# Performance work log

Measured on AMD Instinct MI355X. Metric: run time of the kernel, lower is better.

## Reference

```python
import jax, jax.numpy as jnp
import numpy as np

# D4 Daubechies filter taps (same filter replicated across all channels)
D4 = jnp.array([0.4829629131445341, 0.8365163037378079, 0.2241438680420134, -0.1294095225512604], dtype=jnp.float32)
N_SCALES = 11
SPARSE_DILATIONS = (512, 1024)


def setup_inputs() -> dict:
    key = jax.random.key(0)
    ks = jax.random.split(key, 12)
    B, N, D, H = 4, 4096, 1024, 16
    s = 0.02
    return {
        "x": jax.random.normal(ks[0], (B, N, D), dtype=jnp.float32),
        "Wqkv": jax.random.normal(ks[1], (D, 3 * D), dtype=jnp.float32) * s,
        "bqkv": jnp.zeros((3 * D,), dtype=jnp.float32),
        "Wout": jax.random.normal(ks[2], (D, D), dtype=jnp.float32) * s,
        "bout": jnp.zeros((D,), dtype=jnp.float32),
        "Wgate": jax.random.normal(ks[3], (D, D), dtype=jnp.float32) * s,
        "bgate": jnp.full((D,), 2.0, dtype=jnp.float32),  # nn.init.constant_(bias, 2.0)
        "scale_gain": jax.random.normal(ks[4], (N_SCALES, H), dtype=jnp.float32) * 0.1,
        "skip_w": jnp.full((len(SPARSE_DILATIONS),), -4.0, dtype=jnp.float32)
                  + jax.random.normal(ks[5], (len(SPARSE_DILATIONS),), dtype=jnp.float32) * 0.1,
        "coupling": jnp.eye(H, dtype=jnp.float32)
                    + 0.01 * jax.random.normal(ks[6], (H, H), dtype=jnp.float32),
    }


def _shift_right(t, s, N):
    """Causal shift along seq axis (axis=2): out[i] = t[i-s], zeros for i < s."""
    if s == 0:
        return t
    return jnp.pad(t, ((0, 0), (0, 0), (s, 0), (0, 0)))[:, :, :N, :]


def reference(x, Wqkv, bqkv, Wout, bout, Wgate, bgate, scale_gain, skip_w, coupling):
    B, N, D = x.shape
    H = scale_gain.shape[1]
    HD = D // H

    qkv = x @ Wqkv + bqkv                       # [B, N, 3D]
    q, k, v = jnp.split(qkv, 3, axis=-1)

    def to_heads(t):
        return t.reshape(B, N, H, HD).transpose(0, 2, 1, 3)  # [B, H, N, HD]

    q, k, v = to_heads(q), to_heads(k), to_heads(v)

    k_mag = jnp.linalg.norm(k, axis=-1, keepdims=True)       # [B, H, N, 1]
    field = v * k_mag                                        # [B, H, N, HD]

    # --- 11-scale causal D4 dilated depthwise conv pyramid ---
    # Depthwise conv with identical filter on every channel == weighted sum of
    # causally shifted copies: y[n] = sum_t D4[t] * field[n - (3-t)*d]
    gains = jax.nn.softmax(scale_gain, axis=0)               # [S, H]
    acc = jnp.zeros_like(field)
    for j in range(scale_gain.shape[0]):
        d = 1 << j
        y = sum(D4[t] * _shift_right(field, (3 - t) * d, N) for t in range(4))
        acc = acc + gains[j][None, :, None, None] * y
    field = acc

    # --- sparse long-distance causal skips (1-tap copies at d=512, 1024) ---
    sw = jax.nn.sigmoid(skip_w)
    skip = sum(sw[i] * _shift_right(field, d, N) for i, d in enumerate(SPARSE_DILATIONS))
    field = field + skip

    # --- gated field coupling across heads ---
    coup = jax.nn.softmax(coupling, axis=-1)                 # [H, H]
    field = jnp.einsum('ij,bjnd->bind', coup, field)

    q_flat = q.transpose(0, 2, 1, 3).reshape(B, N, D)
    gate = jax.nn.sigmoid(q_flat @ Wgate + bgate)
    gathered = field.transpose(0, 2, 1, 3).reshape(B, N, D)
    out = (gathered * gate) @ Wout + bout                    # dropout = identity (eval)
    return out
```

## Files before the change

### kernel.cpp

```cpp
#include <hip/hip_runtime.h>
#include <hip/hip_bf16.h>
#include <math.h>

#define BB 4
#define NSEQ 4096
#define DD 1024
#define HH 16
#define HD 64
#define MROWS (BB * NSEQ)

typedef __attribute__((ext_vector_type(8))) short short8;
typedef float v4f __attribute__((ext_vector_type(4)));
typedef unsigned short u16;

typedef __attribute__((address_space(1))) const void gconst_void;
typedef __attribute__((address_space(3))) void lds_void_t;

__device__ __constant__ int SHIFTS[24] = {0,1,2,3,4,6,8,12,16,24,32,48,64,96,128,192,256,384,512,768,1024,1536,2048,3072};

__device__ inline u16 f2bf(float f) {
    unsigned u = __float_as_uint(f);
    unsigned r = u + 0x7fffu + ((u >> 16) & 1u);
    return (u16)(r >> 16);
}
__device__ inline float bf2f(u16 h) {
    return __uint_as_float(((unsigned)h) << 16);
}
__device__ inline void gl2lds16(const u16* g, u16* l) {
    __builtin_amdgcn_global_load_lds((gconst_void*)g, (lds_void_t*)l, 16, 0, 0);
}

__global__ void prep_kernel(const float* __restrict__ scale_gain, const float* __restrict__ skip_w,
                            const float* __restrict__ coupling, float* __restrict__ coefTab,
                            float* __restrict__ coupS, float* __restrict__ swbuf) {
    const float D4T[4] = {0.4829629131445341f, 0.8365163037378079f, 0.2241438680420134f, -0.1294095225512604f};
    int t = threadIdx.x;
    if (t < 2) swbuf[t] = 1.0f / (1.0f + expf(-skip_w[t]));
    if (t < 16) {
        float m = -1e30f;
        for (int j = 0; j < 16; j++) m = fmaxf(m, coupling[t * 16 + j]);
        float s = 0.f, e[16];
        for (int j = 0; j < 16; j++) { e[j] = expf(coupling[t * 16 + j] - m); s += e[j]; }
        for (int j = 0; j < 16; j++) coupS[t * 16 + j] = e[j] / s;
        float g[11];
        m = -1e30f;
        for (int j = 0; j < 11; j++) m = fmaxf(m, scale_gain[j * 16 + t]);
        s = 0.f;
        for (int j = 0; j < 11; j++) { g[j] = expf(scale_gain[j * 16 + t] - m); s += g[j]; }
        for (int j = 0; j < 11; j++) g[j] /= s;
        float cf[24];
        for (int i = 0; i < 24; i++) cf[i] = 0.f;
        for (int j = 0; j < 11; j++) {
            int d = 1 << j;
            for (int tt = 0; tt < 4; tt++) {
                int sh = (3 - tt) * d;
                for (int i = 0; i < 24; i++) {
                    if (SHIFTS[i] == sh) { cf[i] += g[j] * D4T[tt]; break; }
                }
            }
        }
        for (int i = 0; i < 24; i++) coefTab[t * 24 + i] = cf[i];
    }
}

__global__ __launch_bounds__(256) void bfuse_kernel(const float* __restrict__ bqkv, const float* __restrict__ Wgate,
                                                    const float* __restrict__ bgate, float* __restrict__ bfuse) {
    __shared__ float part[4][64];
    int nloc = threadIdx.x & 63, strip = threadIdx.x >> 6;
    int n = blockIdx.x * 64 + nloc;
    float s = 0.f;
    for (int j = strip * 256; j < strip * 256 + 256; j++)
        s += bqkv[j] * Wgate[(long)j * 1024 + n];
    part[strip][nloc] = s;
    __syncthreads();
    if (strip == 0)
        bfuse[n] = bgate[n] + part[0][nloc] + part[1][nloc] + part[2][nloc] + part[3][nloc];
}

__global__ __launch_bounds__(256) void cast_x_kernel(const float* __restrict__ x, u16* __restrict__ xb) {
    long i = ((long)blockIdx.x * 256 + threadIdx.x) * 8;
    float4 f0 = *(const float4*)&x[i];
    float4 f1 = *(const float4*)&x[i + 4];
    u16 o[8];
    o[0] = f2bf(f0.x); o[1] = f2bf(f0.y); o[2] = f2bf(f0.z); o[3] = f2bf(f0.w);
    o[4] = f2bf(f1.x); o[5] = f2bf(f1.y); o[6] = f2bf(f1.z); o[7] = f2bf(f1.w);
    *(uint4*)&xb[i] = *(uint4*)o;
}

__global__ __launch_bounds__(256) void transpose_cast(const float* __restrict__ W, long ldw,
                                                      u16* __restrict__ WT, long ldt) {
    __shared__ float tile[32][33];
    int tx = threadIdx.x, ty = threadIdx.y;
    long x = (long)blockIdx.x * 32 + tx;
    long y0 = (long)blockIdx.y * 32;
    for (int r = 0; r < 32; r += 8)
        tile[ty + r][tx] = W[(y0 + ty + r) * ldw + x];
    __syncthreads();
    for (int r = 0; r < 32; r += 8)
        WT[((long)blockIdx.x * 32 + ty + r) * ldt + y0 + tx] = f2bf(tile[tx][ty + r]);
}

__global__ __launch_bounds__(256) void cast_q_kernel(const float* __restrict__ Wqkv, u16* __restrict__ WqC) {
    long i = ((long)blockIdx.x * 256 + threadIdx.x) * 4;
    int row = (int)(i >> 10);
    int col = (int)(i & 1023);
    float4 f = *(const float4*)&Wqkv[(long)row * 3072 + col];
    ushort4 o;
    o.x = f2bf(f.x); o.y = f2bf(f.y); o.z = f2bf(f.z); o.w = f2bf(f.w);
    *(ushort4*)&WqC[i] = o;
}

#define GEMM_PRE()                                                                  \
    __shared__ u16 As[128 * 32];                                                    \
    __shared__ u16 Bs[128 * 32];                                                    \
    const int tid = threadIdx.x;                                                    \
    const int wave = tid >> 6, lane = tid & 63;                                     \
    const int wm = wave >> 1, wn = wave & 1;                                        \
    const int lrow = lane & 15, kq = lane >> 4;                                     \
    const long m0 = (long)blockIdx.y * 128, n0 = (long)blockIdx.x * 128;            \
    const int r0 = wave * 32 + (lane >> 2);                                         \
    const int sg = (lane & 3) ^ ((r0 >> 1) & 3);                                    \
    const u16* a0 = A + (m0 + r0) * lda + sg * 8;                                   \
    const u16* a1 = a0 + 16 * lda;                                                  \
    const u16* b0 = BT + (n0 + r0) * ldb + sg * 8;                                  \
    const u16* b1 = b0 + 16 * ldb;                                                  \
    u16* la0 = &As[(wave * 32) * 32];                                               \
    u16* la1 = &As[(wave * 32 + 16) * 32];                                          \
    u16* lb0 = &Bs[(wave * 32) * 32];                                               \
    u16* lb1 = &Bs[(wave * 32 + 16) * 32];                                          \
    const int acol = (kq ^ ((lrow >> 1) & 3)) * 8;                                  \
    v4f acc[4][4];                                                                  \
    _Pragma("unroll") for (int i = 0; i < 4; i++)                                   \
        _Pragma("unroll") for (int j = 0; j < 4; j++)                               \
            acc[i][j] = (v4f){0.f, 0.f, 0.f, 0.f};                                  \
    for (int k0 = 0; k0 < K; k0 += 32) {                                            \
        gl2lds16(a0 + k0, la0);                                                     \
        gl2lds16(a1 + k0, la1);                                                     \
        gl2lds16(b0 + k0, lb0);                                                     \
        gl2lds16(b1 + k0, lb1);                                                     \
        __syncthreads();                                                            \
        short8 af[4], bf[4];                                                        \
        _Pragma("unroll") for (int i = 0; i < 4; i++)                               \
            af[i] = *(const short8*)&As[(wm * 64 + i * 16 + lrow) * 32 + acol];     \
        _Pragma("unroll") for (int i = 0; i < 4; i++)                               \
            bf[i] = *(const short8*)&Bs[(wn * 64 + i * 16 + lrow) * 32 + acol];     \
        _Pragma("unroll") for (int im = 0; im < 4; im++)                            \
            _Pragma("unroll") for (int in = 0; in < 4; in++)                        \
                acc[im][in] = __builtin_amdgcn_mfma_f32_16x16x32_bf16(af[im], bf[in], acc[im][in], 0, 0, 0); \
        __syncthreads();                                                            \
    }

template <int CMODE>
__global__ __launch_bounds__(256) void gemm2(const u16* __restrict__ A, long lda,
                                             const u16* __restrict__ BT, long ldb, int K,
                                             const float* __restrict__ bias,
                                             void* __restrict__ Cptr, long ldc) {
    GEMM_PRE()
#pragma unroll
    for (int im = 0; im < 4; im++) {
#pragma unroll
        for (int in = 0; in < 4; in++) {
            long row = m0 + wm * 64 + im * 16 + kq * 4;
            long col = n0 + wn * 64 + in * 16 + lrow;
            float bv = bias ? bias[col] : 0.f;
#pragma unroll
            for (int i = 0; i < 4; i++) {
                float val = acc[im][in][i] + bv;
                long idx = (row + i) * ldc + col;
                if (CMODE == 0) ((float*)Cptr)[idx] = val;
                else            ((u16*)Cptr)[idx] = f2bf(val);
            }
        }
    }
}

#define WAITV(N) asm volatile("s_waitcnt vmcnt(" #N ")" ::: "memory")

template <int CMODE>
__global__ __launch_bounds__(512, 2) void gemm256(const u16* __restrict__ A, long lda,
                                                  const u16* __restrict__ BT, long ldb, int K,
                                                  const float* __restrict__ bias,
                                                  const float* __restrict__ bias2,
                                                  void* __restrict__ C0, void* __restrict__ C1,
                                                  long ldc) {
    __shared__ u16 smem[4 * 2 * 8192];
    const int tid = threadIdx.x;
    const int wv = tid >> 6, lane = tid & 63;
    const int wm = wv >> 2, wn = wv & 3;
    const int lrow = lane & 15, kq = lane >> 4;
    const long m0 = (long)blockIdx.y * 256, n0 = (long)blockIdx.x * 256;

    const int srow = wv * 32 + (lane >> 2);
    const int scol = ((lane & 3) ^ ((lane >> 3) & 3)) * 8;
    const u16* gA0 = A + (m0 + srow) * lda + scol;
    const u16* gA1 = gA0 + 16 * lda;
    const u16* gB0 = BT + (n0 + srow) * ldb + scol;
    const u16* gB1 = gB0 + 16 * ldb;
    const int sb = wv * 32 * 32;

    const int acol = (kq ^ ((lrow >> 1) & 3)) * 8;
    const int aoff = (wm * 128 + lrow) * 32 + acol;
    const int boff = (wn * 64 + lrow) * 32 + acol;

    v4f acc[8][4];
#pragma unroll
    for (int i = 0; i < 8; i++)
#pragma unroll
        for (int j = 0; j < 4; j++) acc[i][j] = (v4f){0.f, 0.f, 0.f, 0.f};

    const int NT = K >> 5;

#define STAGE256(tt) {                                              \
        const int _kk = (tt) << 5;                                  \
        u16* _p = &smem[(((tt) & 3) * 2) * 8192 + sb];              \
        gl2lds16(gA0 + _kk, _p);                                    \
        gl2lds16(gA1 + _kk, _p + 512);                              \
        gl2lds16(gB0 + _kk, _p + 8192);                             \
        gl2lds16(gB1 + _kk, _p + 8192 + 512); }

    STAGE256(0)
    STAGE256(1)
    STAGE256(2)
    WAITV(8);
    __builtin_amdgcn_s_barrier();

    for (int t = 0; t < NT; ++t) {
        if (t + 3 < NT) STAGE256(t + 3)
        const u16* Ab = &smem[((t & 3) * 2) * 8192];
        const u16* Bb = Ab + 8192;
        short8 af[8], bf[4];
#pragma unroll
        for (int i = 0; i < 8; i++) af[i] = *(const short8*)&Ab[aoff + i * 512];
#pragma unroll
        for (int j = 0; j < 4; j++) bf[j] = *(const short8*)&Bb[boff + j * 512];
        __builtin_amdgcn_s_setprio(1);
#pragma unroll
        for (int i = 0; i < 8; i++)
#pragma unroll
            for (int j = 0; j < 4; j++)
                acc[i][j] = __builtin_amdgcn_mfma_f32_16x16x32_bf16(af[i], bf[j], acc[i][j], 0, 0, 0);
        __builtin_amdgcn_s_setprio(0);
        if (t + 3 < NT)      { WAITV(8); }
        else if (t + 2 < NT) { WAITV(4); }
        else if (t + 1 < NT) { WAITV(0); }
        __builtin_amdgcn_s_barrier();
    }
#undef STAGE256

    if (CMODE == 0) {
        float* C = (float*)C0;
#pragma unroll
        for (int im = 0; im < 8; im++) {
#pragma unroll
            for (int in = 0; in < 4; in++) {
                long row = m0 + wm * 128 + im * 16 + kq * 4;
                long col = n0 + wn * 64 + in * 16 + lrow;
                float bv = bias ? bias[col] : 0.f;
#pragma unroll
                for (int i = 0; i < 4; i++)
                    C[(row + i) * ldc + col] = acc[im][in][i] + bv;
            }
        }
    } else {
        u16* kvC = (u16*)C0;
        u16* gateC = (u16*)C1;
        const bool isGate = (n0 >= 2048);
#pragma unroll
        for (int im = 0; im < 8; im++) {
#pragma unroll
            for (int in = 0; in < 4; in++) {
                long row = m0 + wm * 128 + im * 16 + kq * 4;
                long col = n0 + wn * 64 + in * 16 + lrow;
                if (!isGate) {
                    float bv = bias[col];
#pragma unroll
                    for (int i = 0; i < 4; i++)
                        kvC[(row + i) * 2048 + col] = f2bf(acc[im][in][i] + bv);
                } else {
                    long gc = col - 2048;
                    float bv = bias2[gc];
#pragma unroll
                    for (int i = 0; i < 4; i++) {
                        float sgm = 1.0f / (1.0f + expf(-(acc[im][in][i] + bv)));
                        gateC[(row + i) * 1024 + gc] = f2bf(sgm);
                    }
                }
            }
        }
    }
}

__global__ __launch_bounds__(256) void kmag_kernel(const u16* __restrict__ kv, float* __restrict__ kmag) {
    int tid = threadIdx.x;
    int wave = tid >> 6, lane = tid & 63;
    long gid = (long)blockIdx.x * 4 + wave;
    int row = (int)(gid >> 4);
    int h = (int)(gid & 15);
    float kvl = bf2f(kv[(long)row * 2048 + h * 64 + lane]);
    float ss = kvl * kvl;
#pragma unroll
    for (int m = 32; m > 0; m >>= 1) ss += __shfl_xor(ss, m, 64);
    if (lane == 0) {
        int b = row >> 12;
        int n = row & 4095;
        kmag[((long)b * HH + h) * NSEQ + n] = sqrtf(ss);
    }
}

__global__ __launch_bounds__(256) void foldv_kernel(const u16* __restrict__ kv,
                                                    const float* __restrict__ kmag,
                                                    u16* __restrict__ field_t) {
    __shared__ u16 tile[64][72];
    int bh = blockIdx.y;
    int n0 = blockIdx.x * 64;
    int b = bh >> 4, h = bh & 15;
    int t = threadIdx.x;

    {
        int r = t >> 2;
        int c0 = (t & 3) * 16;
        int n = n0 + r;
        const u16* src = kv + ((long)(b * NSEQ + n)) * 2048 + 1024 + h * 64 + c0;
        uint4 u0 = *(const uint4*)src;
        uint4 u1 = *(const uint4*)(src + 8);
        float km = kmag[(long)bh * NSEQ + n];
        u16 in[16], o[16];
        *(uint4*)&in[0] = u0;
        *(uint4*)&in[8] = u1;
#pragma unroll
        for (int i = 0; i < 16; i++) o[i] = f2bf(bf2f(in[i]) * km);
        *(uint4*)&tile[r][c0] = *(uint4*)&o[0];
        *(uint4*)&tile[r][c0 + 8] = *(uint4*)&o[8];
    }
    __syncthreads();

    {
        int cg = t >> 4;
        int q = t & 15;
        u16 o[16];
#pragma unroll
        for (int j = 0; j < 4; j++) {
            int r = q * 4 + j;
            *(ushort4*)&o[j * 4] = *(const ushort4*)&tile[r][cg * 4];
        }
        u16* dst = field_t + (((long)bh * 16 + cg) * NSEQ + n0 + q * 4) * 4;
        *(uint4*)&dst[0] = *(uint4*)&o[0];
        *(uint4*)&dst[8] = *(uint4*)&o[8];
    }
}

__global__ __launch_bounds__(512) void pyramid_kernel(const u16* __restrict__ field_t,
                                                      const float* __restrict__ coefTab,
                                                      u16* __restrict__ accp) {
    __shared__ u16 lds4[NSEQ * 4];
    int blk = blockIdx.x;
    int bh = blk >> 4;
    int cg = blk & 15;
    int hd0 = cg * 4;
    int h = bh & 15;
    int tid = threadIdx.x;

    float cf[24];
#pragma unroll
    for (int i = 0; i < 24; i++) cf[i] = coefTab[h * 24 + i];

    const u16* src = field_t + ((long)bh * 16 + cg) * NSEQ * 4;
#pragma unroll
    for (int k = 0; k < 4; k++) {
        long e = ((long)k * 512 + tid) * 8;
        *(uint4*)&lds4[e] = *(const uint4*)&src[e];
    }
    __syncthreads();

    u16* dst = accp + (long)bh * NSEQ * HD + hd0;
    for (int i = 0; i < 8; i++) {
        int n = tid + i * 512;
        float ax = 0.f, ay = 0.f, az = 0.f, aw = 0.f;
#pragma unroll
        for (int tp = 0; tp < 24; tp++) {
            int s = SHIFTS[tp];
            if (n >= s) {
                const ushort4 f = *(const ushort4*)&lds4[(n - s) * 4];
                float c = cf[tp];
                ax += c * bf2f(f.x); ay += c * bf2f(f.y);
                az += c * bf2f(f.z); aw += c * bf2f(f.w);
            }
        }
        ushort4 o;
        o.x = f2bf(ax); o.y = f2bf(ay); o.z = f2bf(az); o.w = f2bf(aw);
        *(ushort4*)&dst[(long)n * HD] = o;
    }
}

__global__ __launch_bounds__(256) void couple_kernel(const u16* __restrict__ accp,
                                                     const u16* __restrict__ gate,
                                                     const float* __restrict__ coupS,
                                                     const float* __restrict__ swbuf,
                                                     u16* __restrict__ A3) {
    __shared__ float tmp[DD];
    __shared__ float cp[256];
    int row = blockIdx.x;
    int b = row >> 12;
    int n = row & 4095;
    int tid = threadIdx.x;
    float sw0 = swbuf[0], sw1 = swbuf[1];
    cp[tid] = coupS[tid];

    int e = tid * 4;
    int j = e >> 6;
    int hd = e & 63;
    const u16* base = accp + (((long)b * HH + j) * NSEQ + n) * HD + hd;
    ushort4 v0 = *(const ushort4*)base;
    float vx = bf2f(v0.x), vy = bf2f(v0.y), vz = bf2f(v0.z), vw = bf2f(v0.w);
    if (n >= 512) {
        ushort4 s1 = *(const ushort4*)(base - 512 * HD);
        vx += sw0 * bf2f(s1.x); vy += sw0 * bf2f(s1.y);
        vz += sw0 * bf2f(s1.z); vw += sw0 * bf2f(s1.w);
    }
    if (n >= 1024) {
        ushort4 s2 = *(const ushort4*)(base - 1024 * HD);
        vx += sw1 * bf2f(s2.x); vy += sw1 * bf2f(s2.y);
        vz += sw1 * bf2f(s2.z); vw += sw1 * bf2f(s2.w);
    }
    tmp[e] = vx; tmp[e + 1] = vy; tmp[e + 2] = vz; tmp[e + 3] = vw;
    __syncthreads();

    float ox = 0.f, oy = 0.f, oz = 0.f, ow = 0.f;
#pragma unroll
    for (int jj = 0; jj < 16; jj++) {
        float c = cp[j * 16 + jj];
        ox += c * tmp[jj * 64 + hd];
        oy += c * tmp[jj * 64 + hd + 1];
        oz += c * tmp[jj * 64 + hd + 2];
        ow += c * tmp[jj * 64 + hd + 3];
    }
    const ushort4 g = *(const ushort4*)&gate[(long)row * DD + e];
    ox *= bf2f(g.x); oy *= bf2f(g.y); oz *= bf2f(g.z); ow *= bf2f(g.w);
    ushort4 o;
    o.x = f2bf(ox); o.y = f2bf(oy); o.z = f2bf(oz); o.w = f2bf(ow);
    *(ushort4*)&A3[(long)row * DD + e] = o;
}

extern "C" void kernel_launch(void* const* d_in, const int* in_sizes, int n_in,
                              void* d_out, int out_size, void* d_ws, size_t ws_size,
                              hipStream_t stream) {
    const float* x        = (const float*)d_in[0];
    const float* Wqkv     = (const float*)d_in[1];
    const float* bqkv     = (const float*)d_in[2];
    const float* Wout     = (const float*)d_in[3];
    const float* bout     = (const float*)d_in[4];
    const float* Wgate    = (const float*)d_in[5];
    const float* bgate    = (const float*)d_in[6];
    const float* scale_g  = (const float*)d_in[7];
    const float* skip_w   = (const float*)d_in[8];
    const float* coupling = (const float*)d_in[9];

    char* ws = (char*)d_ws;
    size_t off = 0;
    auto alloc = [&](size_t bytes) { char* p = ws + off; off += (bytes + 255) & ~(size_t)255; return p; };

    u16*   kv      = (u16*)alloc((size_t)MROWS * 2048 * 2);
    u16*   gate    = (u16*)alloc((size_t)MROWS * DD * 2);
    u16*   field_t = (u16*)alloc((size_t)BB * HH * NSEQ * HD * 2);
    u16*   WkvT    = (u16*)alloc((size_t)2048 * 1024 * 2);
    u16*   WfuseT  = (u16*)alloc((size_t)1024 * 1024 * 2);
    u16*   WgateT  = (u16*)alloc((size_t)1024 * 1024 * 2);
    u16*   WoutT   = (u16*)alloc((size_t)1024 * 1024 * 2);
    u16*   WqC     = (u16*)alloc((size_t)1024 * 1024 * 2);
    float* kmag    = (float*)alloc((size_t)BB * HH * NSEQ * 4);
    float* bfuse   = (float*)alloc(1024 * 4);
    float* coefT   = (float*)alloc(16 * 24 * 4);
    float* coupS   = (float*)alloc(256 * 4);
    float* swbuf   = (float*)alloc(2 * 4);
    u16*   xb   = field_t;
    u16*   accp = kv;
    u16*   A3   = kv + (size_t)BB * HH * NSEQ * HD;

    cast_x_kernel<<<(MROWS * DD) / (256 * 8), 256, 0, stream>>>(x, xb);

    prep_kernel<<<1, 64, 0, stream>>>(scale_g, skip_w, coupling, coefT, coupS, swbuf);
    bfuse_kernel<<<16, 256, 0, stream>>>(bqkv, Wgate, bgate, bfuse);

    transpose_cast<<<dim3(64, 32), dim3(32, 8), 0, stream>>>(Wqkv + 1024, 3072, WkvT, 1024);
    transpose_cast<<<dim3(32, 32), dim3(32, 8), 0, stream>>>(Wgate, 1024, WgateT, 1024);
    transpose_cast<<<dim3(32, 32), dim3(32, 8), 0, stream>>>(Wout, 1024, WoutT, 1024);
    cast_q_kernel<<<1024, 256, 0, stream>>>(Wqkv, WqC);

    gemm2<1><<<dim3(8, 8), 256, 0, stream>>>(WgateT, 1024, WqC, 1024, 1024,
                                             (const float*)nullptr, WfuseT, 1024);

    gemm256<2><<<dim3(12, 64), 512, 0, stream>>>(xb, 1024, WkvT, 1024, 1024,
                                                 bqkv + 1024, bfuse, kv, gate, 0);

    kmag_kernel<<<(MROWS * HH) / 4, 256, 0, stream>>>(kv, kmag);

    foldv_kernel<<<dim3(64, 64), 256, 0, stream>>>(kv, kmag, field_t);

    pyramid_kernel<<<BB * HH * 16, 512, 0, stream>>>(field_t, coefT, accp);

    couple_kernel<<<MROWS, 256, 0, stream>>>(accp, gate, coupS, swbuf, A3);

    gemm256<0><<<dim3(4, 64), 512, 0, stream>>>(A3, 1024, WoutT, 1024, 1024,
                                                bout, (const float*)nullptr, (float*)d_out, nullptr, 1024);
}
```

Before: 503.8 us.

## Split GEMM main loop into two phases interleaving LDS reads, global loads and MFMA

Restructures the 256x256 GEMM inner loop into two half-phases. Each phase reads part of the A fragments from LDS, issues half of the next-stage global-to-LDS copies (A first, then B), synchronises with barriers and an lgkmcnt wait, then runs half of the MFMAs. This is a ping-pong style schedule meant to overlap memory traffic with matrix math across the two co-resident waves. It adds extra barriers per iteration, which could stall if the interleaving does not pay off.

```diff
diff --git a/kernel.cpp b/kernel.cpp
--- a/kernel.cpp
+++ b/kernel.cpp
@@ -175,6 +175,7 @@
 }
 
 #define WAITV(N) asm volatile("s_waitcnt vmcnt(" #N ")" ::: "memory")
+#define LGKM0()  { asm volatile("s_waitcnt lgkmcnt(0)" ::: "memory"); __builtin_amdgcn_sched_barrier(0); }
 
 template <int CMODE>
 __global__ __launch_bounds__(512, 2) void gemm256(const u16* __restrict__ A, long lda,
@@ -210,32 +211,50 @@
 
     const int NT = K >> 5;
 
-#define STAGE256(tt) {                                              \
+#define STAGE_A(tt) {                                               \
         const int _kk = (tt) << 5;                                  \
         u16* _p = &smem[(((tt) & 3) * 2) * 8192 + sb];              \
         gl2lds16(gA0 + _kk, _p);                                    \
-        gl2lds16(gA1 + _kk, _p + 512);                              \
+        gl2lds16(gA1 + _kk, _p + 512); }
+#define STAGE_B(tt) {                                               \
+        const int _kk = (tt) << 5;                                  \
+        u16* _p = &smem[(((tt) & 3) * 2) * 8192 + sb];              \
         gl2lds16(gB0 + _kk, _p + 8192);                             \
         gl2lds16(gB1 + _kk, _p + 8192 + 512); }
 
-    STAGE256(0)
-    STAGE256(1)
-    STAGE256(2)
+    STAGE_A(0) STAGE_B(0)
+    STAGE_A(1) STAGE_B(1)
+    STAGE_A(2) STAGE_B(2)
     WAITV(8);
     __builtin_amdgcn_s_barrier();
 
     for (int t = 0; t < NT; ++t) {
-        if (t + 3 < NT) STAGE256(t + 3)
         const u16* Ab = &smem[((t & 3) * 2) * 8192];
         const u16* Bb = Ab + 8192;
         short8 af[8], bf[4];
 #pragma unroll
-        for (int i = 0; i < 8; i++) af[i] = *(const short8*)&Ab[aoff + i * 512];
+        for (int i = 0; i < 4; i++) af[i] = *(const short8*)&Ab[aoff + i * 512];
 #pragma unroll
         for (int j = 0; j < 4; j++) bf[j] = *(const short8*)&Bb[boff + j * 512];
+        if (t + 3 < NT) STAGE_A(t + 3)
+        __builtin_amdgcn_s_barrier();
+        LGKM0();
         __builtin_amdgcn_s_setprio(1);
 #pragma unroll
-        for (int i = 0; i < 8; i++)
+        for (int i = 0; i < 4; i++)
+#pragma unroll
+            for (int j = 0; j < 4; j++)
+                acc[i][j] = __builtin_amdgcn_mfma_f32_16x16x32_bf16(af[i], bf[j], acc[i][j], 0, 0, 0);
+        __builtin_amdgcn_s_setprio(0);
+        __builtin_amdgcn_s_barrier();
+#pragma unroll
+        for (int i = 4; i < 8; i++) af[i] = *(const short8*)&Ab[aoff + i * 512];
+        if (t + 3 < NT) STAGE_B(t + 3)
+        __builtin_amdgcn_s_barrier();
+        LGKM0();
+        __builtin_amdgcn_s_setprio(1);
+#pragma unroll
+        for (int i = 4; i < 8; i++)
 #pragma unroll
             for (int j = 0; j < 4; j++)
                 acc[i][j] = __builtin_amdgcn_mfma_f32_16x16x32_bf16(af[i], bf[j], acc[i][j], 0, 0, 0);
@@ -245,7 +264,8 @@
         else if (t + 1 < NT) { WAITV(0); }
         __builtin_amdgcn_s_barrier();
     }
-#undef STAGE256
+#undef STAGE_A
+#undef STAGE_B
 
     if (CMODE == 0) {
         float* C = (float*)C0;
```

New measurement: 520.3 us. +3.3%, slower.

## Fuse k-norm into QKV GEMM epilogue and sparse skips into pyramid

Applied to the files above, without the earlier changes.

Computes the per-head key norm inside the KV GEMM epilogue using wave shuffles, so the separate kmag kernel and its re-read of K go away. Moves the dilated 512/1024 skip taps into the pyramid kernel using rolling registers across its 512-stride loop, which removes two extra bf16 loads per element from the coupling kernel. Replaces the 128-tile weight-fusion GEMM with a 64-tile variant so more workgroups run. The skips now use fp32 pre-rounding values, which changes rounding slightly.

```diff
diff --git a/kernel.cpp b/kernel.cpp
--- a/kernel.cpp
+++ b/kernel.cpp
@@ -110,66 +110,56 @@
     *(ushort4*)&WqC[i] = o;
 }
 
-#define GEMM_PRE()                                                                  \
-    __shared__ u16 As[128 * 32];                                                    \
-    __shared__ u16 Bs[128 * 32];                                                    \
-    const int tid = threadIdx.x;                                                    \
-    const int wave = tid >> 6, lane = tid & 63;                                     \
-    const int wm = wave >> 1, wn = wave & 1;                                        \
-    const int lrow = lane & 15, kq = lane >> 4;                                     \
-    const long m0 = (long)blockIdx.y * 128, n0 = (long)blockIdx.x * 128;            \
-    const int r0 = wave * 32 + (lane >> 2);                                         \
-    const int sg = (lane & 3) ^ ((r0 >> 1) & 3);                                    \
-    const u16* a0 = A + (m0 + r0) * lda + sg * 8;                                   \
-    const u16* a1 = a0 + 16 * lda;                                                  \
-    const u16* b0 = BT + (n0 + r0) * ldb + sg * 8;                                  \
-    const u16* b1 = b0 + 16 * ldb;                                                  \
-    u16* la0 = &As[(wave * 32) * 32];                                               \
-    u16* la1 = &As[(wave * 32 + 16) * 32];                                          \
-    u16* lb0 = &Bs[(wave * 32) * 32];                                               \
-    u16* lb1 = &Bs[(wave * 32 + 16) * 32];                                          \
-    const int acol = (kq ^ ((lrow >> 1) & 3)) * 8;                                  \
-    v4f acc[4][4];                                                                  \
-    _Pragma("unroll") for (int i = 0; i < 4; i++)                                   \
-        _Pragma("unroll") for (int j = 0; j < 4; j++)                               \
-            acc[i][j] = (v4f){0.f, 0.f, 0.f, 0.f};                                  \
-    for (int k0 = 0; k0 < K; k0 += 32) {                                            \
-        gl2lds16(a0 + k0, la0);                                                     \
-        gl2lds16(a1 + k0, la1);                                                     \
-        gl2lds16(b0 + k0, lb0);                                                     \
-        gl2lds16(b1 + k0, lb1);                                                     \
-        __syncthreads();                                                            \
-        short8 af[4], bf[4];                                                        \
-        _Pragma("unroll") for (int i = 0; i < 4; i++)                               \
-            af[i] = *(const short8*)&As[(wm * 64 + i * 16 + lrow) * 32 + acol];     \
-        _Pragma("unroll") for (int i = 0; i < 4; i++)                               \
-            bf[i] = *(const short8*)&Bs[(wn * 64 + i * 16 + lrow) * 32 + acol];     \
-        _Pragma("unroll") for (int im = 0; im < 4; im++)                            \
-            _Pragma("unroll") for (int in = 0; in < 4; in++)                        \
-                acc[im][in] = __builtin_amdgcn_mfma_f32_16x16x32_bf16(af[im], bf[in], acc[im][in], 0, 0, 0); \
-        __syncthreads();                                                            \
-    }
-
-template <int CMODE>
-__global__ __launch_bounds__(256) void gemm2(const u16* __restrict__ A, long lda,
-                                             const u16* __restrict__ BT, long ldb, int K,
-                                             const float* __restrict__ bias,
-                                             void* __restrict__ Cptr, long ldc) {
-    GEMM_PRE()
-#pragma unroll
-    for (int im = 0; im < 4; im++) {
-#pragma unroll
-        for (int in = 0; in < 4; in++) {
-            long row = m0 + wm * 64 + im * 16 + kq * 4;
-            long col = n0 + wn * 64 + in * 16 + lrow;
-            float bv = bias ? bias[col] : 0.f;
-#pragma unroll
-            for (int i = 0; i < 4; i++) {
-                float val = acc[im][in][i] + bv;
-                long idx = (row + i) * ldc + col;
-                if (CMODE == 0) ((float*)Cptr)[idx] = val;
-                else            ((u16*)Cptr)[idx] = f2bf(val);
-            }
+__global__ __launch_bounds__(256) void gemm64(const u16* __restrict__ A, long lda,
+                                              const u16* __restrict__ BT, long ldb, int K,
+                                              u16* __restrict__ C, long ldc) {
+    __shared__ u16 As[64 * 32];
+    __shared__ u16 Bs[64 * 32];
+    const int tid = threadIdx.x;
+    const int wv = tid >> 6, lane = tid & 63;
+    const int wm = wv >> 1, wn = wv & 1;
+    const int lrow = lane & 15, kq = lane >> 4;
+    const long m0 = (long)blockIdx.y * 64, n0 = (long)blockIdx.x * 64;
+
+    const int srow = wv * 16 + (lane >> 2);
+    const int scol = ((lane & 3) ^ ((lane >> 3) & 3)) * 8;
+    const u16* gA = A + (m0 + srow) * lda + scol;
+    const u16* gB = BT + (n0 + srow) * ldb + scol;
+    u16* la = &As[wv * 16 * 32];
+    u16* lb = &Bs[wv * 16 * 32];
+
+    const int acol = (kq ^ ((lrow >> 1) & 3)) * 8;
+    v4f acc[2][2];
+#pragma unroll
+    for (int i = 0; i < 2; i++)
+#pragma unroll
+        for (int j = 0; j < 2; j++) acc[i][j] = (v4f){0.f, 0.f, 0.f, 0.f};
+
+    for (int k0 = 0; k0 < K; k0 += 32) {
+        gl2lds16(gA + k0, la);
+        gl2lds16(gB + k0, lb);
+        __syncthreads();
+        short8 af[2], bf[2];
+#pragma unroll
+        for (int i = 0; i < 2; i++) af[i] = *(const short8*)&As[(wm * 32 + i * 16 + lrow) * 32 + acol];
+#pragma unroll
+        for (int j = 0; j < 2; j++) bf[j] = *(const short8*)&Bs[(wn * 32 + j * 16 + lrow) * 32 + acol];
+#pragma unroll
+        for (int im = 0; im < 2; im++)
+#pragma unroll
+            for (int in = 0; in < 2; in++)
+                acc[im][in] = __builtin_amdgcn_mfma_f32_16x16x32_bf16(af[im], bf[in], acc[im][in], 0, 0, 0);
+        __syncthreads();
+    }
+#pragma unroll
+    for (int im = 0; im < 2; im++) {
+#pragma unroll
+        for (int in = 0; in < 2; in++) {
+            long row = m0 + wm * 32 + im * 16 + kq * 4;
+            long col = n0 + wn * 32 + in * 16 + lrow;
+#pragma unroll
+            for (int i = 0; i < 4; i++)
+                C[(row + i) * ldc + col] = f2bf(acc[im][in][i]);
         }
     }
 }
@@ -182,7 +172,7 @@
                                                   const float* __restrict__ bias,
                                                   const float* __restrict__ bias2,
                                                   void* __restrict__ C0, void* __restrict__ C1,
-                                                  long ldc) {
+                                                  long ldc, float* __restrict__ kmagOut) {
     __shared__ u16 smem[4 * 2 * 8192];
     const int tid = threadIdx.x;
     const int wv = tid >> 6, lane = tid & 63;
@@ -265,19 +255,13 @@
         u16* kvC = (u16*)C0;
         u16* gateC = (u16*)C1;
         const bool isGate = (n0 >= 2048);
-#pragma unroll
-        for (int im = 0; im < 8; im++) {
-#pragma unroll
-            for (int in = 0; in < 4; in++) {
-                long row = m0 + wm * 128 + im * 16 + kq * 4;
-                long col = n0 + wn * 64 + in * 16 + lrow;
-                if (!isGate) {
-                    float bv = bias[col];
-#pragma unroll
-                    for (int i = 0; i < 4; i++)
-                        kvC[(row + i) * 2048 + col] = f2bf(acc[im][in][i] + bv);
-                } else {
-                    long gc = col - 2048;
+        if (isGate) {
+#pragma unroll
+            for (int im = 0; im < 8; im++) {
+#pragma unroll
+                for (int in = 0; in < 4; in++) {
+                    long row = m0 + wm * 128 + im * 16 + kq * 4;
+                    long gc = n0 + wn * 64 + in * 16 + lrow - 2048;
                     float bv = bias2[gc];
 #pragma unroll
                     for (int i = 0; i < 4; i++) {
@@ -286,24 +270,56 @@
                     }
                 }
             }
+        } else if (n0 < 1024) {
+            float bvv[4];
+#pragma unroll
+            for (int in = 0; in < 4; in++) bvv[in] = bias[n0 + wn * 64 + in * 16 + lrow];
+            const int h_g = (int)(n0 >> 6) + wn;
+#pragma unroll
+            for (int im = 0; im < 8; im++) {
+                long row = m0 + wm * 128 + im * 16 + kq * 4;
+                float ss0 = 0.f, ss1 = 0.f, ss2 = 0.f, ss3 = 0.f;
+#pragma unroll
+                for (int in = 0; in < 4; in++) {
+                    long col = n0 + wn * 64 + in * 16 + lrow;
+                    float v0 = acc[im][in][0] + bvv[in];
+                    float v1 = acc[im][in][1] + bvv[in];
+                    float v2 = acc[im][in][2] + bvv[in];
+                    float v3 = acc[im][in][3] + bvv[in];
+                    kvC[(row + 0) * 2048 + col] = f2bf(v0);
+                    kvC[(row + 1) * 2048 + col] = f2bf(v1);
+                    kvC[(row + 2) * 2048 + col] = f2bf(v2);
+                    kvC[(row + 3) * 2048 + col] = f2bf(v3);
+                    ss0 += v0 * v0; ss1 += v1 * v1; ss2 += v2 * v2; ss3 += v3 * v3;
+                }
+#pragma unroll
+                for (int m = 1; m <= 8; m <<= 1) {
+                    ss0 += __shfl_xor(ss0, m, 64);
+                    ss1 += __shfl_xor(ss1, m, 64);
+                    ss2 += __shfl_xor(ss2, m, 64);
+                    ss3 += __shfl_xor(ss3, m, 64);
+                }
+                if (lrow == 0) {
+                    int b = (int)(row >> 12);
+                    int n = (int)(row & 4095);
+                    float4 o4 = make_float4(sqrtf(ss0), sqrtf(ss1), sqrtf(ss2), sqrtf(ss3));
+                    *(float4*)&kmagOut[((long)b * HH + h_g) * NSEQ + n] = o4;
+                }
+            }
+        } else {
+#pragma unroll
+            for (int im = 0; im < 8; im++) {
+#pragma unroll
+                for (int in = 0; in < 4; in++) {
+                    long row = m0 + wm * 128 + im * 16 + kq * 4;
+                    long col = n0 + wn * 64 + in * 16 + lrow;
+                    float bv = bias[col];
+#pragma unroll
+                    for (int i = 0; i < 4; i++)
+                        kvC[(row + i) * 2048 + col] = f2bf(acc[im][in][i] + bv);
+                }
+            }
         }
-    }
-}
-
-__global__ __launch_bounds__(256) void kmag_kernel(const u16* __restrict__ kv, float* __restrict__ kmag) {
-    int tid = threadIdx.x;
-    int wave = tid >> 6, lane = tid & 63;
-    long gid = (long)blockIdx.x * 4 + wave;
-    int row = (int)(gid >> 4);
-    int h = (int)(gid & 15);
-    float kvl = bf2f(kv[(long)row * 2048 + h * 64 + lane]);
-    float ss = kvl * kvl;
-#pragma unroll
-    for (int m = 32; m > 0; m >>= 1) ss += __shfl_xor(ss, m, 64);
-    if (lane == 0) {
-        int b = row >> 12;
-        int n = row & 4095;
-        kmag[((long)b * HH + h) * NSEQ + n] = sqrtf(ss);
     }
 }
 
@@ -351,6 +367,7 @@
 
 __global__ __launch_bounds__(512) void pyramid_kernel(const u16* __restrict__ field_t,
                                                       const float* __restrict__ coefTab,
+                                                      const float* __restrict__ swbuf,
                                                       u16* __restrict__ accp) {
     __shared__ u16 lds4[NSEQ * 4];
     int blk = blockIdx.x;
@@ -363,6 +380,7 @@
     float cf[24];
 #pragma unroll
     for (int i = 0; i < 24; i++) cf[i] = coefTab[h * 24 + i];
+    float sw0 = swbuf[0], sw1 = swbuf[1];
 
     const u16* src = field_t + ((long)bh * 16 + cg) * NSEQ * 4;
 #pragma unroll
@@ -373,6 +391,8 @@
     __syncthreads();
 
     u16* dst = accp + (long)bh * NSEQ * HD + hd0;
+    float p1x = 0.f, p1y = 0.f, p1z = 0.f, p1w = 0.f;
+    float p2x = 0.f, p2y = 0.f, p2z = 0.f, p2w = 0.f;
     for (int i = 0; i < 8; i++) {
         int n = tid + i * 512;
         float ax = 0.f, ay = 0.f, az = 0.f, aw = 0.f;
@@ -386,16 +406,21 @@
                 az += c * bf2f(f.z); aw += c * bf2f(f.w);
             }
         }
+        float ox = ax + sw0 * p1x + sw1 * p2x;
+        float oy = ay + sw0 * p1y + sw1 * p2y;
+        float oz = az + sw0 * p1z + sw1 * p2z;
+        float ow = aw + sw0 * p1w + sw1 * p2w;
         ushort4 o;
-        o.x = f2bf(ax); o.y = f2bf(ay); o.z = f2bf(az); o.w = f2bf(aw);
+        o.x = f2bf(ox); o.y = f2bf(oy); o.z = f2bf(oz); o.w = f2bf(ow);
         *(ushort4*)&dst[(long)n * HD] = o;
+        p2x = p1x; p2y = p1y; p2z = p1z; p2w = p1w;
+        p1x = ax;  p1y = ay;  p1z = az;  p1w = aw;
     }
 }
 
 __global__ __launch_bounds__(256) void couple_kernel(const u16* __restrict__ accp,
                                                      const u16* __restrict__ gate,
                                                      const float* __restrict__ coupS,
-                                                     const float* __restrict__ swbuf,
                                                      u16* __restrict__ A3) {
     __shared__ float tmp[DD];
     __shared__ float cp[256];
@@ -403,7 +428,6 @@
     int b = row >> 12;
     int n = row & 4095;
     int tid = threadIdx.x;
-    float sw0 = swbuf[0], sw1 = swbuf[1];
     cp[tid] = coupS[tid];
 
     int e = tid * 4;
@@ -411,18 +435,8 @@
     int hd = e & 63;
     const u16* base = accp + (((long)b * HH + j) * NSEQ + n) * HD + hd;
     ushort4 v0 = *(const ushort4*)base;
-    float vx = bf2f(v0.x), vy = bf2f(v0.y), vz = bf2f(v0.z), vw = bf2f(v0.w);
-    if (n >= 512) {
-        ushort4 s1 = *(const ushort4*)(base - 512 * HD);
-        vx += sw0 * bf2f(s1.x); vy += sw0 * bf2f(s1.y);
-        vz += sw0 * bf2f(s1.z); vw += sw0 * bf2f(s1.w);
-    }
-    if (n >= 1024) {
-        ushort4 s2 = *(const ushort4*)(base - 1024 * HD);
-        vx += sw1 * bf2f(s2.x); vy += sw1 * bf2f(s2.y);
-        vz += sw1 * bf2f(s2.z); vw += sw1 * bf2f(s2.w);
-    }
-    tmp[e] = vx; tmp[e + 1] = vy; tmp[e + 2] = vz; tmp[e + 3] = vw;
+    tmp[e] = bf2f(v0.x); tmp[e + 1] = bf2f(v0.y);
+    tmp[e + 2] = bf2f(v0.z); tmp[e + 3] = bf2f(v0.w);
     __syncthreads();
 
     float ox = 0.f, oy = 0.f, oz = 0.f, ow = 0.f;
@@ -486,20 +500,18 @@
     transpose_cast<<<dim3(32, 32), dim3(32, 8), 0, stream>>>(Wout, 1024, WoutT, 1024);
     cast_q_kernel<<<1024, 256, 0, stream>>>(Wqkv, WqC);
 
-    gemm2<1><<<dim3(8, 8), 256, 0, stream>>>(WgateT, 1024, WqC, 1024, 1024,
-                                             (const float*)nullptr, WfuseT, 1024);
+    gemm64<<<dim3(16, 16), 256, 0, stream>>>(WgateT, 1024, WqC, 1024, 1024, WfuseT, 1024);
 
     gemm256<2><<<dim3(12, 64), 512, 0, stream>>>(xb, 1024, WkvT, 1024, 1024,
-                                                 bqkv + 1024, bfuse, kv, gate, 0);
-
-    kmag_kernel<<<(MROWS * HH) / 4, 256, 0, stream>>>(kv, kmag);
+                                                 bqkv + 1024, bfuse, kv, gate, 0, kmag);
 
     foldv_kernel<<<dim3(64, 64), 256, 0, stream>>>(kv, kmag, field_t);
 
-    pyramid_kernel<<<BB * HH * 16, 512, 0, stream>>>(field_t, coefT, accp);
-
-    couple_kernel<<<MROWS, 256, 0, stream>>>(accp, gate, coupS, swbuf, A3);
+    pyramid_kernel<<<BB * HH * 16, 512, 0, stream>>>(field_t, coefT, swbuf, accp);
+
+    couple_kernel<<<MROWS, 256, 0, stream>>>(accp, gate, coupS, A3);
 
     gemm256<0><<<dim3(4, 64), 512, 0, stream>>>(A3, 1024, WoutT, 1024, 1024,
-                                                bout, (const float*)nullptr, (float*)d_out, nullptr, 1024);
-}
+                                                bout, (const float*)nullptr, (float*)d_out, nullptr,
+                                                1024, (float*)nullptr);
+}
```

Measured after the change: 458.1 us. -9.1%, faster.
